# Performance work log

Measured on AMD Instinct MI355X. Metric: run time of the kernel, lower is better.

Reference implementation:

```python
import jax, jax.numpy as jnp
import numpy as np

B, LQ, LK, DIM = 2, 2048, 2048, 1024
HEADS, DH = 8, 64
INNER = HEADS * DH  # 512


def setup_inputs() -> dict:
    key = jax.random.key(0)
    ks = jax.random.split(key, 7)
    x = jax.random.normal(ks[0], (B, LQ, DIM), dtype=jnp.float32)
    y = jax.random.normal(ks[1], (B, LK, DIM), dtype=jnp.float32)
    # binary mask, 1 => masked (gets -1e9 added)
    mask = jax.random.randint(ks[2], (B, LQ, LK), 0, 2).astype(jnp.float32)
    s = 0.02
    Wq = jax.random.normal(ks[3], (INNER, DIM), dtype=jnp.float32) * s
    Wk = jax.random.normal(ks[4], (INNER, DIM), dtype=jnp.float32) * s
    Wv = jax.random.normal(ks[5], (INNER, DIM), dtype=jnp.float32) * s
    Wo = jax.random.normal(ks[6], (DIM, INNER), dtype=jnp.float32) * s
    return {"x": x, "y": y, "mask": mask, "Wq": Wq, "Wk": Wk, "Wv": Wv, "Wo": Wo}


def reference(x, y, mask, Wq, Wk, Wv, Wo):
    scale = DH ** -0.5
    # projections (Linear without bias: x @ W.T)
    q = (x @ Wq.T) * scale            # [B, LQ, INNER]
    k = y @ Wk.T                      # [B, LK, INNER]
    v = y @ Wv.T                      # [B, LK, INNER]
    # split into heads (torch.split along last dim == reshape to [.., H, DH])
    q = q.reshape(B, LQ, HEADS, DH)
    k = k.reshape(B, LK, HEADS, DH)
    v = v.reshape(B, LK, HEADS, DH)
    # per-head QK^T + additive mask*-1e9, softmax over keys, then V
    scores = jnp.einsum('bqhd,bkhd->bhqk', q, k) + mask[:, None, :, :] * (-1e9)
    attn = jax.nn.softmax(scores, axis=-1)
    out = jnp.einsum('bhqk,bkhd->bqhd', attn, v).reshape(B, LQ, INNER)
    return out @ Wo.T                 # [B, LQ, DIM]
```

## Files before the change

### kernel.cpp

```cpp
#include <hip/hip_runtime.h>
#include <hip/hip_bf16.h>
#include <stdint.h>

#define BATCH 2
#define LQ 2048
#define LK 2048
#define DIM 1024
#define HEADS 8
#define DH 64
#define INNER 512

typedef __attribute__((ext_vector_type(8))) short short8;
typedef __attribute__((ext_vector_type(4))) float f32x4;
typedef __attribute__((ext_vector_type(16))) float f32x16;

__device__ __forceinline__ float bf2f(unsigned short u) {
    union { unsigned int i; float f; } v;
    v.i = ((unsigned int)u) << 16;
    return v.f;
}
__device__ __forceinline__ unsigned short f2bf(float f) {
    __hip_bfloat16 h = __float2bfloat16(f);
    return *reinterpret_cast<unsigned short*>(&h);
}
__device__ __forceinline__ float fexp2(float x) {
#if __has_builtin(__builtin_amdgcn_exp2f)
    return __builtin_amdgcn_exp2f(x);
#else
    return __expf(x * 0.69314718056f);
#endif
}
__device__ __forceinline__ void stc(unsigned short* C, size_t i, float v) { C[i] = f2bf(v); }
__device__ __forceinline__ void stc(float* C, size_t i, float v) { C[i] = v; }

__device__ __forceinline__ unsigned cvtpk_bf16(float lo, float hi) {
    unsigned r;
    asm("v_cvt_pk_bf16_f32 %0, %1, %2" : "=v"(r) : "v"(lo), "v"(hi));
    return r;
}
__device__ __forceinline__ void perm32swap(unsigned& a, unsigned& b) {
#if __has_builtin(__builtin_amdgcn_permlane32_swap)
    auto r = __builtin_amdgcn_permlane32_swap(a, b, false, false);
    a = r[0]; b = r[1];
#else
    asm volatile("v_permlane32_swap_b32 %0, %1" : "+v"(a), "+v"(b));
#endif
}

typedef __attribute__((address_space(1))) const unsigned int gu32;
typedef __attribute__((address_space(3))) unsigned int lu32;
__device__ __forceinline__ void gload16(const void* g, void* l) {
    __builtin_amdgcn_global_load_lds((gu32*)g, (lu32*)l, 16, 0, 0);
}

__global__ __launch_bounds__(256) void prep(
    const float* __restrict__ x,  const float* __restrict__ y,
    const float* __restrict__ wq, const float* __restrict__ wk,
    const float* __restrict__ wv, const float* __restrict__ wo,
    const float* __restrict__ mask,
    unsigned short* __restrict__ xb,  unsigned short* __restrict__ yb,
    unsigned short* __restrict__ wqb, unsigned short* __restrict__ wkb,
    unsigned short* __restrict__ wvb, unsigned short* __restrict__ wob,
    unsigned long long* __restrict__ mbits)
{
    if (blockIdx.y == 6) {
        const int wid = blockIdx.x * 4 + (threadIdx.x >> 6);
        const int lane = threadIdx.x & 63;
        for (int task = wid; task < BATCH * LQ * 8; task += 4096) {
            int row = task >> 3, g = task & 7;
            const float* mp = mask + (size_t)row * LK + g * 256;
            unsigned long long* ob = mbits + (size_t)row * (LK / 64) + g * 4;
            float v0 = mp[0 * 64 + lane];
            float v1 = mp[1 * 64 + lane];
            float v2 = mp[2 * 64 + lane];
            float v3 = mp[3 * 64 + lane];
            unsigned long long b0 = __ballot(v0 > 0.5f);
            unsigned long long b1 = __ballot(v1 > 0.5f);
            unsigned long long b2 = __ballot(v2 > 0.5f);
            unsigned long long b3 = __ballot(v3 > 0.5f);
            if (lane == 0) { ob[0] = b0; ob[1] = b1; ob[2] = b2; ob[3] = b3; }
        }
        return;
    }
    const float* src; unsigned short* dst; int n4;
    switch (blockIdx.y) {
        case 0: src = x;  dst = xb;  n4 = (BATCH * LQ * DIM) / 4; break;
        case 1: src = y;  dst = yb;  n4 = (BATCH * LK * DIM) / 4; break;
        case 2: src = wq; dst = wqb; n4 = (INNER * DIM) / 4; break;
        case 3: src = wk; dst = wkb; n4 = (INNER * DIM) / 4; break;
        case 4: src = wv; dst = wvb; n4 = (INNER * DIM) / 4; break;
        default: src = wo; dst = wob; n4 = (INNER * DIM) / 4; break;
    }
    const int stride = gridDim.x * 256;
    for (int i = blockIdx.x * 256 + threadIdx.x; i < n4; i += stride) {
        float4 f = ((const float4*)src)[i];
        ushort4 u;
        u.x = f2bf(f.x); u.y = f2bf(f.y); u.z = f2bf(f.z); u.w = f2bf(f.w);
        ((ushort4*)dst)[i] = u;
    }
}

template <int IM, int JN, int WR, int WC, typename TC, int EPI>
__device__ __forceinline__ void gemm_body(
    const unsigned short* __restrict__ A,
    const unsigned short* __restrict__ W,
    TC* __restrict__ C,
    int K, int N, float scale,
    unsigned short* SH)
{
    constexpr int THREADS = WR * WC * 64;
    constexpr int BM = WR * IM * 16;
    constexpr int BN = WC * JN * 16;
    constexpr int ACH = BM * 8;
    constexpr int BCH = BN * 8;
    constexpr int AUS = BM * 64;
    constexpr int BUS = BN * 64;

    unsigned short* As = SH;
    unsigned short* Bs = SH + 2 * AUS;

    const int tid = threadIdx.x;
    const int m0 = blockIdx.x * BM;
    const int n0 = blockIdx.y * BN;
    const int w = tid >> 6, lane = tid & 63;
    const int q4 = lane >> 4, l16 = lane & 15;
    const int wm = (w / WC) * (IM * 16), wn = (w % WC) * (JN * 16);
    const int sw = l16 & 7;

    f32x4 acc[IM][JN] = {};

#pragma unroll
    for (int i = 0; i < ACH / THREADS; ++i) {
        int s = tid + i * THREADS;
        int r = s >> 3, ch = (s & 7) ^ (r & 7);
        gload16(A + (size_t)(m0 + r) * K + ch * 8, As + (size_t)s * 8);
    }
#pragma unroll
    for (int i = 0; i < BCH / THREADS; ++i) {
        int s = tid + i * THREADS;
        int r = s >> 3, ch = (s & 7) ^ (r & 7);
        gload16(W + (size_t)(n0 + r) * K + ch * 8, Bs + (size_t)s * 8);
    }
    __syncthreads();

    const int nt = K / 64;
    for (int t = 0; t < nt; ++t) {
        const int curA = (t & 1) * AUS;
        const int curB = (t & 1) * BUS;
        if (t + 1 < nt) {
            int kk = (t + 1) * 64;
            const int nxtA = AUS - curA, nxtB = BUS - curB;
#pragma unroll
            for (int i = 0; i < ACH / THREADS; ++i) {
                int s = tid + i * THREADS;
                int r = s >> 3, ch = (s & 7) ^ (r & 7);
                gload16(A + (size_t)(m0 + r) * K + kk + ch * 8, As + nxtA + (size_t)s * 8);
            }
#pragma unroll
            for (int i = 0; i < BCH / THREADS; ++i) {
                int s = tid + i * THREADS;
                int r = s >> 3, ch = (s & 7) ^ (r & 7);
                gload16(W + (size_t)(n0 + r) * K + kk + ch * 8, Bs + nxtB + (size_t)s * 8);
            }
        }

#pragma unroll
        for (int ks = 0; ks < 2; ++ks) {
            const int kq = ((ks * 4 + q4) ^ sw) * 8;
            short8 a[IM], b[JN];
#pragma unroll
            for (int i = 0; i < IM; ++i)
                a[i] = *(const short8*)(As + curA + (wm + i * 16 + l16) * 64 + kq);
#pragma unroll
            for (int j = 0; j < JN; ++j)
                b[j] = *(const short8*)(Bs + curB + (wn + j * 16 + l16) * 64 + kq);
#pragma unroll
            for (int i = 0; i < IM; ++i)
#pragma unroll
                for (int j = 0; j < JN; ++j)
                    acc[i][j] = __builtin_amdgcn_mfma_f32_16x16x32_bf16(
                        a[i], b[j], acc[i][j], 0, 0, 0);
        }
        __syncthreads();
    }

    if (EPI == 0) {
#pragma unroll
        for (int i = 0; i < IM; ++i)
#pragma unroll
            for (int j = 0; j < JN; ++j)
#pragma unroll
                for (int r = 0; r < 4; ++r) {
                    int row = m0 + wm + i * 16 + q4 * 4 + r;
                    int col = n0 + wn + j * 16 + l16;
                    stc(C, (size_t)row * N + col, acc[i][j][r] * scale);
                }
    } else {
        constexpr int KW = IM * 16;
        constexpr int DW = JN * 16;
        constexpr int TPS = KW + 8;
        unsigned short* TP = SH + w * (DW * TPS);
#pragma unroll
        for (int i = 0; i < IM; ++i)
#pragma unroll
            for (int j = 0; j < JN; ++j) {
                ushort4 u;
                u.x = f2bf(acc[i][j][0]); u.y = f2bf(acc[i][j][1]);
                u.z = f2bf(acc[i][j][2]); u.w = f2bf(acc[i][j][3]);
                *(ushort4*)(TP + (j * 16 + l16) * TPS + i * 16 + q4 * 4) = u;
            }
        const int keyflat = m0 + wm;
        const int bb = keyflat >> 11, key0 = keyflat & (LK - 1);
        const int hh = (n0 + wn) >> 6;
        const int dlow = (n0 + wn) & 63;
        constexpr int RCH = KW / 8;
        constexpr int NCH = DW * RCH;
#pragma unroll
        for (int p = 0; p < NCH / 64; ++p) {
            int c = p * 64 + lane;
            int dl = c / RCH, kc = c % RCH;
            uint4 v = *(const uint4*)(TP + dl * TPS + kc * 8);
            *(uint4*)((unsigned short*)C +
                ((size_t)((bb * HEADS + hh) * DH + dlow + dl)) * LK + key0 + kc * 8) = v;
        }
    }
}

#define QSCALE 0.18033688011112042f

__global__ __launch_bounds__(512) void proj_qkv(
    const unsigned short* __restrict__ xb, const unsigned short* __restrict__ yb,
    const unsigned short* __restrict__ wqb, const unsigned short* __restrict__ wkb,
    const unsigned short* __restrict__ wvb,
    unsigned short* __restrict__ qb, unsigned short* __restrict__ kb,
    unsigned short* __restrict__ vt)
{
    __shared__ __align__(16) unsigned short SH[4 * 128 * 64];
    const int z = blockIdx.z;
    const unsigned short* A = (z == 0) ? xb : yb;
    const unsigned short* W = (z == 0) ? wqb : (z == 1) ? wkb : wvb;
    if (z == 2)
        gemm_body<4, 2, 2, 4, unsigned short, 1>(A, W, vt, DIM, INNER, 1.0f, SH);
    else
        gemm_body<4, 2, 2, 4, unsigned short, 0>(A, W, (z == 0) ? qb : kb, DIM, INNER,
                                                 (z == 0) ? QSCALE : 1.0f, SH);
}

__global__ __launch_bounds__(512) void gemm_out(
    const unsigned short* __restrict__ A,
    const unsigned short* __restrict__ W,
    float* __restrict__ C)
{
    __shared__ __align__(16) unsigned short SH[4 * 128 * 64];
    gemm_body<4, 2, 2, 4, float, 0>(A, W, C, INNER, DIM, 1.0f, SH);
}

#define AT_SLOT (64 * 64)

__global__ __launch_bounds__(512, 4) void attn_mfma(
    const unsigned short* __restrict__ Q,
    const unsigned short* __restrict__ Kb,
    const unsigned short* __restrict__ Vt,
    const unsigned long long* __restrict__ Mb,
    unsigned short* __restrict__ O)
{
    __shared__ __align__(16) unsigned short Ks[4 * AT_SLOT];
    __shared__ __align__(16) unsigned short Vs[4 * AT_SLOT];

    const int tid = threadIdx.x;
    const int L = blockIdx.x;
    const int h = L & 7;
    const int jj = L >> 3;
    const int b = jj >> 5;
    const int q0 = (jj & 31) * 64;
    const int w = tid >> 6, lane = tid & 63;
    const int qh = w & 1;
    const int kh = (w >> 1) & 1;
    const int par = w >> 2;
    const int l31 = lane & 31, hl = lane >> 5;

    short8 qf[4];
    {
        const unsigned short* qp =
            Q + (size_t)(b * LQ + q0 + qh * 32 + l31) * INNER + h * DH + 8 * hl;
#pragma unroll
        for (int ks = 0; ks < 4; ++ks)
            qf[ks] = *(const short8*)(qp + ks * 16);
    }

    f32x16 o[2] = {};
    float lacc = 0.f;

    const unsigned short* kbase = Kb + (size_t)(b * LK) * INNER + h * DH;
    const unsigned short* vbase = Vt + (size_t)((b * HEADS + h) * DH) * LK;
    const unsigned long long* mrow =
        Mb + (size_t)(b * LQ + q0 + qh * 32 + l31) * (LK / 64);

    const int rr = tid >> 3;
    const int ch = (tid & 7) ^ (rr & 7);

#pragma unroll
    for (int tn = 0; tn < 2; ++tn) {
        gload16(kbase + (size_t)(tn * 64 + rr) * INNER + ch * 8,
                Ks + tn * AT_SLOT + (size_t)tid * 8);
        gload16(vbase + (size_t)rr * LK + tn * 64 + ch * 8,
                Vs + tn * AT_SLOT + (size_t)tid * 8);
    }
    __syncthreads();

    const int l7 = lane & 7;
    const int NR = LK / 128;
    for (int rd = 0; rd < NR; ++rd) {
        if (rd + 1 < NR) {
#pragma unroll
            for (int i = 0; i < 2; ++i) {
                const int tn = 2 * rd + 2 + i;
                const int sl = tn & 3;
                gload16(kbase + (size_t)(tn * 64 + rr) * INNER + ch * 8,
                        Ks + sl * AT_SLOT + (size_t)tid * 8);
                gload16(vbase + (size_t)rr * LK + tn * 64 + ch * 8,
                        Vs + sl * AT_SLOT + (size_t)tid * 8);
            }
        }
        const int t = 2 * rd + par;
        const int cur = (t & 3) * AT_SLOT;

        f32x16 s = {};
        __builtin_amdgcn_s_setprio(1);
#pragma unroll
        for (int ks = 0; ks < 4; ++ks) {
            const int R = kh * 32 + l31;
            const int c0 = ks * 2 + hl;
            short8 kf = *(const short8*)(Ks + cur + R * 64 + ((c0 ^ l7) * 8));
            s = __builtin_amdgcn_mfma_f32_32x32x16_bf16(kf, qf[ks], s, 0, 0, 0);
        }
        __builtin_amdgcn_s_setprio(0);

        unsigned bits32 = (unsigned)(mrow[t] >> (kh * 32));
        unsigned pk[8];
#pragma unroll
        for (int g = 0; g < 4; ++g) {
            unsigned nib = (bits32 >> (8 * g + 4 * hl)) & 0xFu;
            float p0 = (nib & 1u) ? 0.f : fexp2(s[4 * g + 0]);
            float p1 = (nib & 2u) ? 0.f : fexp2(s[4 * g + 1]);
            float p2 = (nib & 4u) ? 0.f : fexp2(s[4 * g + 2]);
            float p3 = (nib & 8u) ? 0.f : fexp2(s[4 * g + 3]);
            lacc += (p0 + p1) + (p2 + p3);
            pk[2 * g]     = cvtpk_bf16(p0, p1);
            pk[2 * g + 1] = cvtpk_bf16(p2, p3);
        }

        short8 pf[2];
#pragma unroll
        for (int k2 = 0; k2 < 2; ++k2) {
            unsigned r0 = pk[4 * k2 + 0], r2 = pk[4 * k2 + 2];
            unsigned r1 = pk[4 * k2 + 1], r3 = pk[4 * k2 + 3];
            perm32swap(r0, r2);
            perm32swap(r1, r3);
            union { unsigned u[4]; short8 s8; } up;
            up.u[0] = r0; up.u[1] = r1; up.u[2] = r2; up.u[3] = r3;
            pf[k2] = up.s8;
        }

        __builtin_amdgcn_s_setprio(1);
#pragma unroll
        for (int df = 0; df < 2; ++df) {
#pragma unroll
            for (int k2 = 0; k2 < 2; ++k2) {
                const int R = df * 32 + l31;
                const int c0 = kh * 4 + k2 * 2 + hl;
                short8 vf = *(const short8*)(Vs + cur + R * 64 + ((c0 ^ l7) * 8));
                o[df] = __builtin_amdgcn_mfma_f32_32x32x16_bf16(vf, pf[k2], o[df], 0, 0, 0);
            }
        }
        __builtin_amdgcn_s_setprio(0);
        __syncthreads();
    }

    float* xq = (float*)(qh ? (void*)Vs : (void*)Ks);
    const int wslot = par * 2 + kh;
    if (wslot) {
        float* d = xq + (size_t)((wslot - 1) * 64 + lane) * 33;
#pragma unroll
        for (int df = 0; df < 2; ++df)
#pragma unroll
            for (int r = 0; r < 16; ++r) d[df * 16 + r] = o[df][r];
        d[32] = lacc;
    }
    __syncthreads();
    if (!wslot) {
#pragma unroll
        for (int ws2 = 0; ws2 < 3; ++ws2) {
            const float* d = xq + (size_t)(ws2 * 64 + lane) * 33;
#pragma unroll
            for (int df = 0; df < 2; ++df)
#pragma unroll
                for (int r = 0; r < 16; ++r) o[df][r] += d[df * 16 + r];
            lacc += d[32];
        }
        lacc += __shfl_xor(lacc, 32);
        const float inv = 1.0f / lacc;

        unsigned short* orow =
            O + (size_t)(b * LQ + q0 + qh * 32 + l31) * INNER + h * DH;
#pragma unroll
        for (int df = 0; df < 2; ++df)
#pragma unroll
            for (int g = 0; g < 4; ++g) {
                ushort4 u;
                u.x = f2bf(o[df][4 * g + 0] * inv);
                u.y = f2bf(o[df][4 * g + 1] * inv);
                u.z = f2bf(o[df][4 * g + 2] * inv);
                u.w = f2bf(o[df][4 * g + 3] * inv);
                *(ushort4*)(orow + df * 32 + 8 * g + 4 * hl) = u;
            }
    }
}

extern "C" void kernel_launch(void* const* d_in, const int* in_sizes, int n_in,
                              void* d_out, int out_size, void* d_ws, size_t ws_size,
                              hipStream_t stream) {
    const float* x    = (const float*)d_in[0];
    const float* y    = (const float*)d_in[1];
    const float* mask = (const float*)d_in[2];
    const float* Wq   = (const float*)d_in[3];
    const float* Wk   = (const float*)d_in[4];
    const float* Wv   = (const float*)d_in[5];
    const float* Wo   = (const float*)d_in[6];
    float* out = (float*)d_out;

    const size_t NX = (size_t)BATCH * LQ * DIM;
    const size_t NS = (size_t)BATCH * LQ * INNER;
    const size_t NW = (size_t)INNER * DIM;
    unsigned short* xb  = (unsigned short*)d_ws;
    unsigned short* yb  = xb + NX;
    unsigned short* qb  = yb + NX;
    unsigned short* kb  = qb + NS;
    unsigned short* vt  = kb + NS;
    unsigned short* wqb = vt + NS;
    unsigned short* wkb = wqb + NW;
    unsigned short* wvb = wkb + NW;
    unsigned short* wob = wvb + NW;
    unsigned long long* mbits = (unsigned long long*)(wob + NW);
    unsigned short* ao  = xb;

    dim3 blk(256);
    prep<<<dim3(1024, 7), blk, 0, stream>>>(
        x, y, Wq, Wk, Wv, Wo, mask, xb, yb, wqb, wkb, wvb, wob, mbits);
    proj_qkv<<<dim3(4096 / 128, INNER / 128, 3), dim3(512), 0, stream>>>(
        xb, yb, wqb, wkb, wvb, qb, kb, vt);
    attn_mfma<<<dim3(512), dim3(512), 0, stream>>>(
        qb, kb, vt, mbits, ao);
    gemm_out<<<dim3(4096 / 128, DIM / 128), dim3(512), 0, stream>>>(ao, wob, out);
}
```

Before: 174.0 us.

## Halve attention block size and load V fragments directly from global memory

The attention kernel now uses 256-thread blocks that each cover 32 query rows, launched as 1024 blocks, so each block holds a single query half. The V tile is no longer staged in shared memory; each wave reads its V MFMA operands straight from global (L2) memory, and only K is double-buffered in LDS, whose footprint is halved. The aim is lower LDS use and higher occupancy, at the cost of uncoalesced 16-byte V reads from global memory and K tiles being reloaded by twice as many blocks.

Measured after the change: 191.8 us. +10.2%, slower.

```diff
diff --git a/kernel.cpp b/kernel.cpp
--- a/kernel.cpp
+++ b/kernel.cpp
@@ -255,34 +255,33 @@
     gemm_body<4, 2, 2, 4, float, 0>(A, W, C, INNER, DIM, 1.0f, SH);
 }
 
-#define AT_SLOT (64 * 64)
-
-__global__ __launch_bounds__(512, 4) void attn_mfma(
+#define KSLOT (64 * 64)
+
+__global__ __launch_bounds__(256, 4) void attn_mfma(
     const unsigned short* __restrict__ Q,
     const unsigned short* __restrict__ Kb,
     const unsigned short* __restrict__ Vt,
     const unsigned long long* __restrict__ Mb,
     unsigned short* __restrict__ O)
 {
-    __shared__ __align__(16) unsigned short Ks[4 * AT_SLOT];
-    __shared__ __align__(16) unsigned short Vs[4 * AT_SLOT];
+    __shared__ __align__(16) unsigned short Ks[4 * KSLOT];
 
     const int tid = threadIdx.x;
     const int L = blockIdx.x;
     const int h = L & 7;
     const int jj = L >> 3;
-    const int b = jj >> 5;
-    const int q0 = (jj & 31) * 64;
+    const int b = jj >> 6;
+    const int q0 = (jj & 63) * 32;
     const int w = tid >> 6, lane = tid & 63;
-    const int qh = w & 1;
-    const int kh = (w >> 1) & 1;
-    const int par = w >> 2;
+    const int kh = w & 1;
+    const int par = w >> 1;
     const int l31 = lane & 31, hl = lane >> 5;
+    const int l7 = lane & 7;
 
     short8 qf[4];
     {
         const unsigned short* qp =
-            Q + (size_t)(b * LQ + q0 + qh * 32 + l31) * INNER + h * DH + 8 * hl;
+            Q + (size_t)(b * LQ + q0 + l31) * INNER + h * DH + 8 * hl;
 #pragma unroll
         for (int ks = 0; ks < 4; ++ks)
             qf[ks] = *(const short8*)(qp + ks * 16);
@@ -294,21 +293,21 @@
     const unsigned short* kbase = Kb + (size_t)(b * LK) * INNER + h * DH;
     const unsigned short* vbase = Vt + (size_t)((b * HEADS + h) * DH) * LK;
     const unsigned long long* mrow =
-        Mb + (size_t)(b * LQ + q0 + qh * 32 + l31) * (LK / 64);
-
-    const int rr = tid >> 3;
-    const int ch = (tid & 7) ^ (rr & 7);
+        Mb + (size_t)(b * LQ + q0 + l31) * (LK / 64);
+
+    const int r0 = tid >> 3, ch0 = (tid & 7) ^ (r0 & 7);
+    const int s1 = tid + 256;
+    const int r1 = s1 >> 3, ch1 = (s1 & 7) ^ (r1 & 7);
 
 #pragma unroll
     for (int tn = 0; tn < 2; ++tn) {
-        gload16(kbase + (size_t)(tn * 64 + rr) * INNER + ch * 8,
-                Ks + tn * AT_SLOT + (size_t)tid * 8);
-        gload16(vbase + (size_t)rr * LK + tn * 64 + ch * 8,
-                Vs + tn * AT_SLOT + (size_t)tid * 8);
+        gload16(kbase + (size_t)(tn * 64 + r0) * INNER + ch0 * 8,
+                Ks + tn * KSLOT + (size_t)tid * 8);
+        gload16(kbase + (size_t)(tn * 64 + r1) * INNER + ch1 * 8,
+                Ks + tn * KSLOT + (size_t)s1 * 8);
     }
     __syncthreads();
 
-    const int l7 = lane & 7;
     const int NR = LK / 128;
     for (int rd = 0; rd < NR; ++rd) {
         if (rd + 1 < NR) {
@@ -316,14 +315,23 @@
             for (int i = 0; i < 2; ++i) {
                 const int tn = 2 * rd + 2 + i;
                 const int sl = tn & 3;
-                gload16(kbase + (size_t)(tn * 64 + rr) * INNER + ch * 8,
-                        Ks + sl * AT_SLOT + (size_t)tid * 8);
-                gload16(vbase + (size_t)rr * LK + tn * 64 + ch * 8,
-                        Vs + sl * AT_SLOT + (size_t)tid * 8);
+                gload16(kbase + (size_t)(tn * 64 + r0) * INNER + ch0 * 8,
+                        Ks + sl * KSLOT + (size_t)tid * 8);
+                gload16(kbase + (size_t)(tn * 64 + r1) * INNER + ch1 * 8,
+                        Ks + sl * KSLOT + (size_t)s1 * 8);
             }
         }
         const int t = 2 * rd + par;
-        const int cur = (t & 3) * AT_SLOT;
+        const int cur = (t & 3) * KSLOT;
+
+        short8 vf[2][2];
+#pragma unroll
+        for (int df = 0; df < 2; ++df)
+#pragma unroll
+            for (int k2 = 0; k2 < 2; ++k2)
+                vf[df][k2] = *(const short8*)(vbase
+                    + (size_t)(df * 32 + l31) * LK + t * 64
+                    + (kh * 4 + k2 * 2 + hl) * 8);
 
         f32x16 s = {};
         __builtin_amdgcn_s_setprio(1);
@@ -353,34 +361,30 @@
         short8 pf[2];
 #pragma unroll
         for (int k2 = 0; k2 < 2; ++k2) {
-            unsigned r0 = pk[4 * k2 + 0], r2 = pk[4 * k2 + 2];
-            unsigned r1 = pk[4 * k2 + 1], r3 = pk[4 * k2 + 3];
-            perm32swap(r0, r2);
-            perm32swap(r1, r3);
+            unsigned r0u = pk[4 * k2 + 0], r2u = pk[4 * k2 + 2];
+            unsigned r1u = pk[4 * k2 + 1], r3u = pk[4 * k2 + 3];
+            perm32swap(r0u, r2u);
+            perm32swap(r1u, r3u);
             union { unsigned u[4]; short8 s8; } up;
-            up.u[0] = r0; up.u[1] = r1; up.u[2] = r2; up.u[3] = r3;
+            up.u[0] = r0u; up.u[1] = r1u; up.u[2] = r2u; up.u[3] = r3u;
             pf[k2] = up.s8;
         }
 
         __builtin_amdgcn_s_setprio(1);
 #pragma unroll
-        for (int df = 0; df < 2; ++df) {
-#pragma unroll
-            for (int k2 = 0; k2 < 2; ++k2) {
-                const int R = df * 32 + l31;
-                const int c0 = kh * 4 + k2 * 2 + hl;
-                short8 vf = *(const short8*)(Vs + cur + R * 64 + ((c0 ^ l7) * 8));
-                o[df] = __builtin_amdgcn_mfma_f32_32x32x16_bf16(vf, pf[k2], o[df], 0, 0, 0);
-            }
-        }
+        for (int df = 0; df < 2; ++df)
+#pragma unroll
+            for (int k2 = 0; k2 < 2; ++k2)
+                o[df] = __builtin_amdgcn_mfma_f32_32x32x16_bf16(
+                    vf[df][k2], pf[k2], o[df], 0, 0, 0);
         __builtin_amdgcn_s_setprio(0);
         __syncthreads();
     }
 
-    float* xq = (float*)(qh ? (void*)Vs : (void*)Ks);
+    float* xch = (float*)Ks;
     const int wslot = par * 2 + kh;
     if (wslot) {
-        float* d = xq + (size_t)((wslot - 1) * 64 + lane) * 33;
+        float* d = xch + (size_t)((wslot - 1) * 64 + lane) * 33;
 #pragma unroll
         for (int df = 0; df < 2; ++df)
 #pragma unroll
@@ -391,7 +395,7 @@
     if (!wslot) {
 #pragma unroll
         for (int ws2 = 0; ws2 < 3; ++ws2) {
-            const float* d = xq + (size_t)(ws2 * 64 + lane) * 33;
+            const float* d = xch + (size_t)(ws2 * 64 + lane) * 33;
 #pragma unroll
             for (int df = 0; df < 2; ++df)
 #pragma unroll
@@ -402,7 +406,7 @@
         const float inv = 1.0f / lacc;
 
         unsigned short* orow =
-            O + (size_t)(b * LQ + q0 + qh * 32 + l31) * INNER + h * DH;
+            O + (size_t)(b * LQ + q0 + l31) * INNER + h * DH;
 #pragma unroll
         for (int df = 0; df < 2; ++df)
 #pragma unroll
@@ -449,7 +453,7 @@
         x, y, Wq, Wk, Wv, Wo, mask, xb, yb, wqb, wkb, wvb, wob, mbits);
     proj_qkv<<<dim3(4096 / 128, INNER / 128, 3), dim3(512), 0, stream>>>(
         xb, yb, wqb, wkb, wvb, qb, kb, vt);
-    attn_mfma<<<dim3(512), dim3(512), 0, stream>>>(
+    attn_mfma<<<dim3(1024), dim3(256), 0, stream>>>(
         qb, kb, vt, mbits, ao);
     gemm_out<<<dim3(4096 / 128, DIM / 128), dim3(512), 0, stream>>>(ao, wob, out);
 }
```
